# Kernel tuning notes

Measured on AMD Instinct MI355X. Metric: run time of the kernel, lower is better.

The kernel has to match this reference:

```python
import jax, jax.numpy as jnp
import numpy as np

EPS = 1e-5  # equinox LayerNorm default eps

def setup_inputs() -> dict:
    key = jax.random.key(0)
    k1, k2, k3, k4, k5 = jax.random.split(key, 5)
    heads, d, dH, N = 16, 1024, 64, 2048
    # lecun-normal-ish scaling for fan_in=d
    s = 1.0 / np.sqrt(d)
    return {
        "x": jax.random.normal(k1, (d, N), dtype=jnp.float32),
        "WQ": jax.random.normal(k2, (heads, d, dH), dtype=jnp.float32) * s,
        "WK": jax.random.normal(k3, (heads, d, dH), dtype=jnp.float32) * s,
        "WV": jax.random.normal(k4, (heads, d, dH), dtype=jnp.float32) * s,
        "W0": jax.random.normal(k5, (d, d), dtype=jnp.float32) * s,
    }

def reference(x, WQ, WK, WV, W0):
    # x: [d, N]
    residual = x
    # equinox LayerNorm over full shape (d, N), no affine params
    mean = jnp.mean(x)
    var = jnp.var(x)
    xn = (x - mean) * jax.lax.rsqrt(var + EPS)
    # project: [h, d_model, dH] x [d_model, N] -> [h, dH, N]
    Q = jnp.einsum('hcd,ci->hdi', WQ, xn)
    K = jnp.einsum('hcd,ci->hdi', WK, xn)
    V = jnp.einsum('hcd,ci->hdi', WV, xn)
    dH = WK.shape[-1]
    dot = jnp.einsum('hdi,hdj->hij', Q, K)  # [h, N, N]
    alpha = jax.nn.softmax(dot / jnp.sqrt(jnp.asarray(dH, dot.dtype)), axis=-1)
    attn = jnp.einsum('hij,hdj->hdi', alpha, V)  # [h, dH, N]
    N = attn.shape[2]
    attn = attn.reshape(-1, N)  # [d, N]
    out = W0 @ attn
    return out + residual
```

## Files before the change

kernel.cpp:

```cpp
#include <hip/hip_runtime.h>
#include <math.h>

typedef unsigned short u16;
typedef _Float16 f16;
typedef __attribute__((ext_vector_type(8))) short bf16x8;
typedef __attribute__((ext_vector_type(4))) float f32x4;
typedef __attribute__((ext_vector_type(4))) f16 f16x4;

#define D_MODEL 1024
#define SEQ_N   2048
#define HEADS   16
#define DHEAD   64
#define M3      3072
#define NIT     (SEQ_N / 64)
#define QSCALE  0.18033688011112042f
#define EXPOFF  5.770780163555854f

#define GLOBAL_AS __attribute__((address_space(1)))
#define LDS_AS    __attribute__((address_space(3)))
#define ASYNC16(gp, lp) __builtin_amdgcn_global_load_lds( \
    (const GLOBAL_AS unsigned int*)(gp), (LDS_AS unsigned int*)(lp), 16, 0, 0)

__device__ __forceinline__ u16 f2bf(float f) {
  union { float f; unsigned int u; } v; v.f = f;
  unsigned int r = v.u + 0x7fffu + ((v.u >> 16) & 1u);
  return (u16)(r >> 16);
}

__global__ __launch_bounds__(256) void prep(const float* __restrict__ x,
                                            double* __restrict__ part,
                                            const float* __restrict__ WQ,
                                            const float* __restrict__ WK,
                                            const float* __restrict__ WV,
                                            const float* __restrict__ W0,
                                            u16* __restrict__ Wp,
                                            u16* __restrict__ W0p) {
  __shared__ double ls[256], lss[256];
  __shared__ float tile[32][65];
  int t = threadIdx.x;
  int b = blockIdx.x;
  if (b < 256) {
    const float4* x4 = (const float4*)x;
    const int n4 = (D_MODEL * SEQ_N) / 4;
    double s = 0.0, ss = 0.0;
    for (int idx = b * 256 + t; idx < n4; idx += 256 * 256) {
      float4 v = x4[idx];
      s  += (double)v.x + (double)v.y + (double)v.z + (double)v.w;
      ss += (double)v.x * v.x + (double)v.y * v.y + (double)v.z * v.z + (double)v.w * v.w;
    }
    ls[t] = s; lss[t] = ss;
    __syncthreads();
    for (int off = 128; off > 0; off >>= 1) {
      if (t < off) { ls[t] += ls[t + off]; lss[t] += lss[t + off]; }
      __syncthreads();
    }
    if (t == 0) { part[2 * b] = ls[0]; part[2 * b + 1] = lss[0]; }
    return;
  }
  int f = b - 256;
  int z = f >> 9;
  int rem = f & 511;
  if (z == 3) {
    int idx = rem * 512 + t;
#pragma unroll
    for (int r = 0; r < 2; ++r, idx += 256) {
      float4 v = ((const float4*)W0)[idx];
      unsigned int lo = (unsigned int)f2bf(v.x) | ((unsigned int)f2bf(v.y) << 16);
      unsigned int hi = (unsigned int)f2bf(v.z) | ((unsigned int)f2bf(v.w) << 16);
      uint2 o; o.x = lo; o.y = hi;
      *(uint2*)(&W0p[(size_t)idx * 4]) = o;
    }
    return;
  }
  const float* W = (z == 0) ? WQ : ((z == 1) ? WK : WV);
  int h = rem >> 5, cb = (rem & 31) * 32;
  int dh = t & 63, cl = t >> 6;
  for (int r = 0; r < 8; ++r) {
    int c = cl + r * 4;
    tile[c][dh] = W[((size_t)h * D_MODEL + cb + c) * DHEAD + dh];
  }
  __syncthreads();
  int c2 = t & 31, d2 = t >> 5;
  for (int r = 0; r < 8; ++r) {
    int dd = d2 + r * 8;
    Wp[(size_t)((z * HEADS + h) * DHEAD + dd) * D_MODEL + cb + c2] = f2bf(tile[c2][dd]);
  }
}

__global__ __launch_bounds__(256) void ln_norm_t(const float* __restrict__ x,
                                                 const double* __restrict__ part,
                                                 u16* __restrict__ xnt) {
  __shared__ double ls[256], lss[256];
  __shared__ float tile[64][65];
  int t = threadIdx.x;
  ls[t] = part[2 * t]; lss[t] = part[2 * t + 1];
  __syncthreads();
  for (int off = 128; off > 0; off >>= 1) {
    if (t < off) { ls[t] += ls[t + off]; lss[t] += lss[t + off]; }
    __syncthreads();
  }
  double inv = 1.0 / ((double)D_MODEL * (double)SEQ_N);
  double m = ls[0] * inv;
  double vv = lss[0] * inv - m * m;
  float mean = (float)m;
  float rstd = (float)(1.0 / sqrt(vv + 1e-5));

  int ib = blockIdx.x * 64, cb = blockIdx.y * 64;
  int il = t & 63, cl = t >> 6;
  for (int r = 0; r < 16; ++r) {
    int c = cl + r * 4;
    tile[c][il] = (x[(size_t)(cb + c) * SEQ_N + ib + il] - mean) * rstd;
  }
  __syncthreads();
  int c2 = t & 63, i2 = t >> 6;
  for (int r = 0; r < 16; ++r) {
    int i = i2 + r * 4;
    xnt[(size_t)(ib + i) * D_MODEL + cb + c2] = f2bf(tile[c2][i]);
  }
}

__global__ __launch_bounds__(256) void gemm_qkv(const u16* __restrict__ A,
                                                const u16* __restrict__ Bt,
                                                u16* __restrict__ Qt,
                                                u16* __restrict__ Kt,
                                                f16* __restrict__ Vb) {
  __shared__ __align__(16) u16 Alds[2 * 2 * 96 * 32];
  __shared__ __align__(16) u16 Blds[2 * 2 * 128 * 32];
  int t = threadIdx.x;
  int lane = t & 63, w = t >> 6;
  int g = lane >> 4, l16 = lane & 15;
  int wr = w >> 1, wc = w & 1;
  int flat = blockIdx.x;
  int wi = flat >> 3;
  int wx = wi & 7, wy = wi >> 3;
  int cx = (flat & 7) & 1, cy = (flat & 7) >> 1;
  int bx = cx * 8 + wx;
  int by = cy * 8 + wy;
  int mb = by * 96, nb = bx * 128;

  f32x4 acc[3][4];
#pragma unroll
  for (int i = 0; i < 3; ++i)
#pragma unroll
    for (int j = 0; j < 4; ++j) acc[i][j] = (f32x4){0.f, 0.f, 0.f, 0.f};

  const u16* AgP[3]; int ldsA[3];
#pragma unroll
  for (int r = 0; r < 3; ++r) {
    int idx = r * 256 + t;
    int kk = (idx >= 384) ? 1 : 0;
    int rem = idx - kk * 384;
    int row = rem >> 2, c4 = rem & 3;
    int csw = c4 ^ ((row >> 1) & 3);
    AgP[r] = A + (size_t)(mb + row) * D_MODEL + kk * 32 + csw * 8;
    ldsA[r] = idx * 8;
  }
  const u16* BgP[4]; int ldsB[4];
#pragma unroll
  for (int r = 0; r < 4; ++r) {
    int idx = r * 256 + t;
    int kk = idx >> 9;
    int rem = idx & 511;
    int row = rem >> 2, c4 = rem & 3;
    int csw = c4 ^ ((row >> 1) & 3);
    BgP[r] = Bt + (size_t)(nb + row) * D_MODEL + kk * 32 + csw * 8;
    ldsB[r] = idx * 8;
  }

#pragma unroll
  for (int r = 0; r < 3; ++r) ASYNC16(AgP[r], &Alds[ldsA[r]]);
#pragma unroll
  for (int r = 0; r < 4; ++r) ASYNC16(BgP[r], &Blds[ldsB[r]]);
#pragma unroll
  for (int r = 0; r < 3; ++r) ASYNC16(AgP[r] + 64, &Alds[6144 + ldsA[r]]);
#pragma unroll
  for (int r = 0; r < 4; ++r) ASYNC16(BgP[r] + 64, &Blds[8192 + ldsB[r]]);

  int rowa0 = wr * 48, rowb0 = wc * 64;
  int cur = 0;
  for (int ks = 0; ks < 16; ++ks) {
    if (ks < 15) asm volatile("s_waitcnt vmcnt(7)" ::: "memory");
    else         asm volatile("s_waitcnt vmcnt(0)" ::: "memory");
    __builtin_amdgcn_s_barrier();
#pragma unroll
    for (int kk = 0; kk < 2; ++kk) {
      bf16x8 af[3], bf[4];
#pragma unroll
      for (int tm = 0; tm < 3; ++tm) {
        int row = rowa0 + tm * 16 + l16;
        int gs = g ^ ((row >> 1) & 3);
        af[tm] = *(const bf16x8*)(&Alds[cur * 6144 + kk * 3072 + row * 32 + gs * 8]);
      }
#pragma unroll
      for (int tn = 0; tn < 4; ++tn) {
        int row = rowb0 + tn * 16 + l16;
        int gs = g ^ ((row >> 1) & 3);
        bf[tn] = *(const bf16x8*)(&Blds[cur * 8192 + kk * 4096 + row * 32 + gs * 8]);
      }
#pragma unroll
      for (int tm = 0; tm < 3; ++tm)
#pragma unroll
        for (int tn = 0; tn < 4; ++tn)
          acc[tm][tn] = __builtin_amdgcn_mfma_f32_16x16x32_bf16(af[tm], bf[tn],
                                                                acc[tm][tn], 0, 0, 0);
    }
    __builtin_amdgcn_s_barrier();
    if (ks + 2 < 16) {
      int kb = (ks + 2) * 64;
#pragma unroll
      for (int r = 0; r < 3; ++r) ASYNC16(AgP[r] + kb, &Alds[cur * 6144 + ldsA[r]]);
#pragma unroll
      for (int r = 0; r < 4; ++r) ASYNC16(BgP[r] + kb, &Blds[cur * 8192 + ldsB[r]]);
    }
    cur ^= 1;
  }

#pragma unroll
  for (int tm = 0; tm < 3; ++tm) {
    int row0 = mb + wr * 48 + tm * 16 + g * 4;
#pragma unroll
    for (int tn = 0; tn < 4; ++tn) {
      int col = nb + wc * 64 + tn * 16 + l16;
      if (row0 < 2 * D_MODEL) {
        u16* T = (row0 < D_MODEL) ? Qt : Kt;
        float sc = (row0 < D_MODEL) ? QSCALE : 1.0f;
        int rbase = (row0 < D_MODEL) ? row0 : row0 - D_MODEL;
        ushort4 o;
        o.x = f2bf(acc[tm][tn][0] * sc); o.y = f2bf(acc[tm][tn][1] * sc);
        o.z = f2bf(acc[tm][tn][2] * sc); o.w = f2bf(acc[tm][tn][3] * sc);
        *(ushort4*)(&T[(size_t)col * D_MODEL + rbase]) = o;
      } else {
        int rbase = row0 - 2 * D_MODEL;
#pragma unroll
        for (int r = 0; r < 4; ++r)
          Vb[(size_t)(rbase + r) * SEQ_N + col] = (f16)acc[tm][tn][r];
      }
    }
  }
}

__global__ __launch_bounds__(256) void gemm_bf16(const u16* __restrict__ A,
                                                 const u16* __restrict__ Bt,
                                                 float* __restrict__ C,
                                                 const float* __restrict__ res,
                                                 int M, int N, int K) {
  __shared__ __align__(16) u16 Alds[2 * 2 * 64 * 32];
  __shared__ __align__(16) u16 Blds[2 * 2 * 64 * 32];
  int t = threadIdx.x;
  int w = t >> 6, lane = t & 63;
  int g = lane >> 4, l16 = lane & 15;
  int flat = blockIdx.x;
  int wi = flat >> 3;
  int wx = wi & 7, wy = wi >> 3;
  int cx = (flat & 7) & 3, cy = (flat & 7) >> 2;
  int bx = cx * 8 + wx;
  int by = cy * 8 + wy;
  int mb = by * 64, nb = bx * 64;
  f32x4 acc[4];
  for (int i = 0; i < 4; ++i) acc[i] = (f32x4){0.f, 0.f, 0.f, 0.f};

  const u16* AgP[2]; const u16* BgP[2]; int ldsO[2];
#pragma unroll
  for (int r = 0; r < 2; ++r) {
    int idx = r * 256 + t;
    int kk = idx >> 8;
    int rem = idx & 255;
    int row = rem >> 2, c4 = rem & 3;
    int csw = c4 ^ ((row >> 1) & 3);
    AgP[r] = A + (size_t)(mb + row) * K + kk * 32 + csw * 8;
    BgP[r] = Bt + (size_t)(nb + row) * K + kk * 32 + csw * 8;
    ldsO[r] = idx * 8;
  }

#pragma unroll
  for (int r = 0; r < 2; ++r) { ASYNC16(AgP[r], &Alds[ldsO[r]]); ASYNC16(BgP[r], &Blds[ldsO[r]]); }
#pragma unroll
  for (int r = 0; r < 2; ++r) {
    ASYNC16(AgP[r] + 64, &Alds[4096 + ldsO[r]]);
    ASYNC16(BgP[r] + 64, &Blds[4096 + ldsO[r]]);
  }

  int cur = 0;
  const int NK = 16;
  for (int ks = 0; ks < NK; ++ks) {
    if (ks < NK - 1) asm volatile("s_waitcnt vmcnt(4)" ::: "memory");
    else             asm volatile("s_waitcnt vmcnt(0)" ::: "memory");
    __builtin_amdgcn_s_barrier();
#pragma unroll
    for (int kk = 0; kk < 2; ++kk) {
      int rowa = w * 16 + l16;
      int gsa = g ^ ((rowa >> 1) & 3);
      bf16x8 af = *(const bf16x8*)(&Alds[cur * 4096 + kk * 2048 + rowa * 32 + gsa * 8]);
#pragma unroll
      for (int tn = 0; tn < 4; ++tn) {
        int rowb = tn * 16 + l16;
        int gsb = g ^ ((rowb >> 1) & 3);
        bf16x8 bf = *(const bf16x8*)(&Blds[cur * 4096 + kk * 2048 + rowb * 32 + gsb * 8]);
        acc[tn] = __builtin_amdgcn_mfma_f32_16x16x32_bf16(af, bf, acc[tn], 0, 0, 0);
      }
    }
    __builtin_amdgcn_s_barrier();
    if (ks + 2 < NK) {
      int kb = (ks + 2) * 64;
#pragma unroll
      for (int r = 0; r < 2; ++r) {
        ASYNC16(AgP[r] + kb, &Alds[cur * 4096 + ldsO[r]]);
        ASYNC16(BgP[r] + kb, &Blds[cur * 4096 + ldsO[r]]);
      }
    }
    cur ^= 1;
  }
  int col0 = nb + l16;
  int row0 = mb + w * 16 + g * 4;
#pragma unroll
  for (int tn = 0; tn < 4; ++tn) {
    int col = col0 + tn * 16;
#pragma unroll
    for (int r = 0; r < 4; ++r) {
      int row = row0 + r;
      float v = acc[tn][r];
      if (res) v += res[(size_t)row * N + col];
      C[(size_t)row * N + col] = v;
    }
  }
}

#define KSW(buf_, row_, ch_) ((buf_)*4096 + (row_)*64 + ((((ch_) ^ ((row_)&7)))*8))
__global__ __launch_bounds__(256, 2) void attn_mfma(const u16* __restrict__ Qt,
                                                    const u16* __restrict__ Kt,
                                                    const f16* __restrict__ Vb,
                                                    u16* __restrict__ attnt) {
  __shared__ __align__(16) u16 Klds[2 * 64 * 64];
  __shared__ __align__(16) f16 Vlds[2 * 64 * 64];
  int flat = blockIdx.x;
  int xcd = flat & 7, idx = flat >> 3;
  int h  = xcd * 2 + (idx >> 5);
  int ib = (idx & 31) * 64;
  int t = threadIdx.x;
  int w = t >> 6, lane = t & 63;
  int g = lane >> 4, l16 = lane & 15;

  bf16x8 bq[2];
  {
    const u16* qb = Qt + (size_t)(ib + w * 16 + l16) * D_MODEL + h * DHEAD + g * 8;
    bq[0] = *(const bf16x8*)(qb);
    bq[1] = *(const bf16x8*)(qb + 32);
  }

  f32x4 acc_o[4];
#pragma unroll
  for (int i = 0; i < 4; ++i) acc_o[i] = (f32x4){0.f, 0.f, 0.f, 0.f};
  f32x4 acc_l = (f32x4){0.f, 0.f, 0.f, 0.f};
  f16x4 ones;
  ones[0] = (f16)1.f; ones[1] = (f16)1.f; ones[2] = (f16)1.f; ones[3] = (f16)1.f;

  int srow = t >> 2, sc0 = (t & 3) * 16;
  int c0 = (t & 3) * 2;
  const u16* Kg = Kt + (size_t)srow * D_MODEL + h * DHEAD + sc0;
  const f16* Vg = Vb + (size_t)(h * DHEAD + srow) * SEQ_N + sc0;

  uint4 ka = *(const uint4*)(Kg);
  uint4 kb = *(const uint4*)(Kg + 8);
  uint4 va = *(const uint4*)(Vg);
  uint4 vb = *(const uint4*)(Vg + 8);
  *(uint4*)(&Klds[KSW(0, srow, c0)])     = ka;
  *(uint4*)(&Klds[KSW(0, srow, c0 + 1)]) = kb;
  *(uint4*)(&Vlds[KSW(0, srow, c0)])     = va;
  *(uint4*)(&Vlds[KSW(0, srow, c0 + 1)]) = vb;
  __syncthreads();

  int cur = 0;
  for (int it = 0; it < NIT; ++it) {
    if (it + 1 < NIT) {
      const u16* Kn = Kg + (size_t)(it + 1) * 64 * D_MODEL;
      const f16* Vn = Vg + (it + 1) * 64;
      ka = *(const uint4*)(Kn);
      kb = *(const uint4*)(Kn + 8);
      va = *(const uint4*)(Vn);
      vb = *(const uint4*)(Vn + 8);
    }

    f32x4 s[4];
#pragma unroll
    for (int i = 0; i < 4; ++i) s[i] = (f32x4){0.f, 0.f, 0.f, 0.f};
    __builtin_amdgcn_s_setprio(1);
#pragma unroll
    for (int kk = 0; kk < 2; ++kk)
#pragma unroll
      for (int tn = 0; tn < 4; ++tn) {
        int row = tn * 16 + l16;
        bf16x8 ak = *(const bf16x8*)(&Klds[KSW(cur, row, kk * 4 + g)]);
        s[tn] = __builtin_amdgcn_mfma_f32_16x16x32_bf16(ak, bq[kk], s[tn], 0, 0, 0);
      }
    __builtin_amdgcn_s_setprio(0);
    f16x4 pf[4];
#pragma unroll
    for (int tn = 0; tn < 4; ++tn) {
      f16x4 p;
#pragma unroll
      for (int r = 0; r < 4; ++r)
        p[r] = (f16)exp2f(s[tn][r] - EXPOFF);
      pf[tn] = p;
    }
    __builtin_amdgcn_s_setprio(1);
#pragma unroll
    for (int tn = 0; tn < 4; ++tn) {
      acc_l = __builtin_amdgcn_mfma_f32_16x16x16f16(pf[tn], ones, acc_l, 0, 0, 0);
#pragma unroll
      for (int td = 0; td < 4; ++td) {
        int row = td * 16 + l16;
        f16x4 bv = *(const f16x4*)(&Vlds[KSW(cur, row, tn * 2 + (g >> 1)) + (g & 1) * 4]);
        acc_o[td] =
            __builtin_amdgcn_mfma_f32_16x16x16f16(pf[tn], bv, acc_o[td], 0, 0, 0);
      }
    }
    __builtin_amdgcn_s_setprio(0);

    if (it + 1 < NIT) {
      *(uint4*)(&Klds[KSW(cur ^ 1, srow, c0)])     = ka;
      *(uint4*)(&Klds[KSW(cur ^ 1, srow, c0 + 1)]) = kb;
      *(uint4*)(&Vlds[KSW(cur ^ 1, srow, c0)])     = va;
      *(uint4*)(&Vlds[KSW(cur ^ 1, srow, c0 + 1)]) = vb;
    }
    __syncthreads();
    cur ^= 1;
  }

  float inv0 = 1.0f / acc_l[0];
  float inv1 = 1.0f / acc_l[1];
  float inv2 = 1.0f / acc_l[2];
  float inv3 = 1.0f / acc_l[3];
#pragma unroll
  for (int td = 0; td < 4; ++td) {
    int dh = h * DHEAD + td * 16 + l16;
    int i0 = ib + w * 16 + g * 4;
    attnt[(size_t)(i0 + 0) * D_MODEL + dh] = f2bf(acc_o[td][0] * inv0);
    attnt[(size_t)(i0 + 1) * D_MODEL + dh] = f2bf(acc_o[td][1] * inv1);
    attnt[(size_t)(i0 + 2) * D_MODEL + dh] = f2bf(acc_o[td][2] * inv2);
    attnt[(size_t)(i0 + 3) * D_MODEL + dh] = f2bf(acc_o[td][3] * inv3);
  }
}

extern "C" void kernel_launch(void* const* d_in, const int* in_sizes, int n_in,
                              void* d_out, int out_size, void* d_ws, size_t ws_size,
                              hipStream_t stream) {
  const float* x  = (const float*)d_in[0];
  const float* WQ = (const float*)d_in[1];
  const float* WK = (const float*)d_in[2];
  const float* WV = (const float*)d_in[3];
  const float* W0 = (const float*)d_in[4];
  float* out = (float*)d_out;

  char* ws = (char*)d_ws;
  size_t off = 0;
  double* part  = (double*)(ws + off); off += 8192;
  u16*    xnt   = (u16*)(ws + off); off += (size_t)SEQ_N * D_MODEL * 2;
  u16*    Wp    = (u16*)(ws + off); off += (size_t)M3 * D_MODEL * 2;
  u16*    W0p   = (u16*)(ws + off); off += (size_t)D_MODEL * D_MODEL * 2;
  u16*    Qt    = (u16*)(ws + off); off += (size_t)SEQ_N * D_MODEL * 2;
  u16*    Kt    = (u16*)(ws + off); off += (size_t)SEQ_N * D_MODEL * 2;
  f16*    Vb    = (f16*)(ws + off); off += (size_t)D_MODEL * SEQ_N * 2;
  u16*    attnt = (u16*)(ws + off); off += (size_t)SEQ_N * D_MODEL * 2;

  prep<<<256 + 2048, 256, 0, stream>>>(x, part, WQ, WK, WV, W0, Wp, W0p);
  ln_norm_t<<<dim3(SEQ_N / 64, D_MODEL / 64), 256, 0, stream>>>(x, part, xnt);
  gemm_qkv<<<512, 256, 0, stream>>>(Wp, xnt, Qt, Kt, Vb);
  attn_mfma<<<512, 256, 0, stream>>>(Qt, Kt, Vb, attnt);
  gemm_bf16<<<512, 256, 0, stream>>>(W0p, attnt, out, x, D_MODEL, SEQ_N, D_MODEL);
}
```

Measured before the change: 153.5 us.

## Split attention over key chunks and add a combine kernel

Splits the attention key/value sequence into two chunks, doubling the attention grid. Each block writes unnormalized fp16 partial outputs and fp32 row sums. A new combine kernel adds the partials, normalizes them and writes the bf16 attention output for the output projection. The aim is more parallel blocks in the attention stage. The cost is extra workspace traffic, one more kernel launch, and a possible fp16 range or precision risk in the unnormalized partials.

```diff
diff --git a/kernel.cpp b/kernel.cpp
--- a/kernel.cpp
+++ b/kernel.cpp
@@ -12,7 +12,9 @@
 #define HEADS   16
 #define DHEAD   64
 #define M3      3072
-#define NIT     (SEQ_N / 64)
+#define JSPLIT  2
+#define JCHUNK  (SEQ_N / JSPLIT)
+#define NIT     (JCHUNK / 64)
 #define QSCALE  0.18033688011112042f
 #define EXPOFF  5.770780163555854f
 
@@ -329,13 +331,16 @@
 __global__ __launch_bounds__(256, 2) void attn_mfma(const u16* __restrict__ Qt,
                                                     const u16* __restrict__ Kt,
                                                     const f16* __restrict__ Vb,
-                                                    u16* __restrict__ attnt) {
+                                                    f16* __restrict__ Opart,
+                                                    float* __restrict__ Lpart) {
   __shared__ __align__(16) u16 Klds[2 * 64 * 64];
   __shared__ __align__(16) f16 Vlds[2 * 64 * 64];
   int flat = blockIdx.x;
   int xcd = flat & 7, idx = flat >> 3;
-  int h  = xcd * 2 + (idx >> 5);
+  int h  = xcd * 2 + ((idx >> 5) & 1);
+  int sp = idx >> 6;
   int ib = (idx & 31) * 64;
+  int j0 = sp * JCHUNK;
   int t = threadIdx.x;
   int w = t >> 6, lane = t & 63;
   int g = lane >> 4, l16 = lane & 15;
@@ -356,8 +361,8 @@
 
   int srow = t >> 2, sc0 = (t & 3) * 16;
   int c0 = (t & 3) * 2;
-  const u16* Kg = Kt + (size_t)srow * D_MODEL + h * DHEAD + sc0;
-  const f16* Vg = Vb + (size_t)(h * DHEAD + srow) * SEQ_N + sc0;
+  const u16* Kg = Kt + (size_t)(j0 + srow) * D_MODEL + h * DHEAD + sc0;
+  const f16* Vg = Vb + (size_t)(h * DHEAD + srow) * SEQ_N + j0 + sc0;
 
   uint4 ka = *(const uint4*)(Kg);
   uint4 kb = *(const uint4*)(Kg + 8);
@@ -426,19 +431,44 @@
     cur ^= 1;
   }
 
-  float inv0 = 1.0f / acc_l[0];
-  float inv1 = 1.0f / acc_l[1];
-  float inv2 = 1.0f / acc_l[2];
-  float inv3 = 1.0f / acc_l[3];
+  if (l16 == 0) {
+#pragma unroll
+    for (int r = 0; r < 4; ++r)
+      Lpart[((size_t)sp * HEADS + h) * SEQ_N + ib + w * 16 + g * 4 + r] = acc_l[r];
+  }
+
 #pragma unroll
   for (int td = 0; td < 4; ++td) {
     int dh = h * DHEAD + td * 16 + l16;
-    int i0 = ib + w * 16 + g * 4;
-    attnt[(size_t)(i0 + 0) * D_MODEL + dh] = f2bf(acc_o[td][0] * inv0);
-    attnt[(size_t)(i0 + 1) * D_MODEL + dh] = f2bf(acc_o[td][1] * inv1);
-    attnt[(size_t)(i0 + 2) * D_MODEL + dh] = f2bf(acc_o[td][2] * inv2);
-    attnt[(size_t)(i0 + 3) * D_MODEL + dh] = f2bf(acc_o[td][3] * inv3);
-  }
+#pragma unroll
+    for (int r = 0; r < 4; ++r) {
+      int i = ib + w * 16 + g * 4 + r;
+      Opart[((size_t)sp * SEQ_N + i) * D_MODEL + dh] = (f16)acc_o[td][r];
+    }
+  }
+}
+
+__global__ __launch_bounds__(256) void attn_combine(const f16* __restrict__ Opart,
+                                                    const float* __restrict__ Lpart,
+                                                    u16* __restrict__ attnt) {
+  int i = blockIdx.x;
+  int c = threadIdx.x * 4;
+  int h = c >> 6;
+  float l = 0.f;
+#pragma unroll
+  for (int s = 0; s < JSPLIT; ++s) l += Lpart[((size_t)s * HEADS + h) * SEQ_N + i];
+  float o[4] = {0.f, 0.f, 0.f, 0.f};
+#pragma unroll
+  for (int s = 0; s < JSPLIT; ++s) {
+    f16x4 v = *(const f16x4*)(&Opart[((size_t)s * SEQ_N + i) * D_MODEL + c]);
+#pragma unroll
+    for (int r = 0; r < 4; ++r) o[r] += (float)v[r];
+  }
+  float inv = 1.0f / l;
+  ushort4 ob;
+  ob.x = f2bf(o[0] * inv); ob.y = f2bf(o[1] * inv);
+  ob.z = f2bf(o[2] * inv); ob.w = f2bf(o[3] * inv);
+  *(ushort4*)(&attnt[(size_t)i * D_MODEL + c]) = ob;
 }
 
 extern "C" void kernel_launch(void* const* d_in, const int* in_sizes, int n_in,
@@ -461,10 +491,13 @@
   u16*    Kt    = (u16*)(ws + off); off += (size_t)SEQ_N * D_MODEL * 2;
   f16*    Vb    = (f16*)(ws + off); off += (size_t)D_MODEL * SEQ_N * 2;
   u16*    attnt = (u16*)(ws + off); off += (size_t)SEQ_N * D_MODEL * 2;
+  f16*    Opart = (f16*)(ws + off); off += (size_t)JSPLIT * SEQ_N * D_MODEL * 2;
+  float*  Lpart = (float*)(ws + off); off += (size_t)JSPLIT * HEADS * SEQ_N * 4;
 
   prep<<<256 + 2048, 256, 0, stream>>>(x, part, WQ, WK, WV, W0, Wp, W0p);
   ln_norm_t<<<dim3(SEQ_N / 64, D_MODEL / 64), 256, 0, stream>>>(x, part, xnt);
   gemm_qkv<<<512, 256, 0, stream>>>(Wp, xnt, Qt, Kt, Vb);
-  attn_mfma<<<512, 256, 0, stream>>>(Qt, Kt, Vb, attnt);
+  attn_mfma<<<1024, 256, 0, stream>>>(Qt, Kt, Vb, Opart, Lpart);
+  attn_combine<<<SEQ_N, 256, 0, stream>>>(Opart, Lpart, attnt);
   gemm_bf16<<<512, 256, 0, stream>>>(W0p, attnt, out, x, D_MODEL, SEQ_N, D_MODEL);
 }
```

After: 153.7 us. About the same (+0.2%).
